# Performance work log

Measured on AMD Instinct MI355X. Metric: run time of the kernel, lower is better.

The kernel has to match this reference:

```python
import jax, jax.numpy as jnp
import numpy as np

N_NODES = 100000
N_EDGES = 3200000
D_IN = 128
UNITS = 128


def setup_inputs() -> dict:
    key = jax.random.key(0)
    k1, k2, k3, k4, k5, k6 = jax.random.split(key, 6)
    x = jax.random.normal(k1, (N_NODES, D_IN), dtype=jnp.float32)
    edge_src = jax.random.randint(k2, (N_EDGES,), 0, N_NODES, dtype=jnp.int32)
    edge_dst = jax.random.randint(k3, (N_EDGES,), 0, N_NODES, dtype=jnp.int32)
    edge_vals = jax.random.uniform(k4, (N_EDGES,), dtype=jnp.float32)
    w = jax.random.normal(k5, (D_IN, UNITS), dtype=jnp.float32) * (2.0 / D_IN) ** 0.5  # he_normal scale
    b = jax.random.normal(k6, (UNITS,), dtype=jnp.float32) * 0.05
    return {"x": x, "edge_src": edge_src, "edge_dst": edge_dst,
            "edge_vals": edge_vals, "w": w, "b": b}


def reference(x, edge_src, edge_dst, edge_vals, w, b):
    # dense transform: [N, D_IN] @ [D_IN, UNITS] -> [N, UNITS]
    h = x @ w
    # sparse adjacency SpMM via edge list: out[dst] += val * h[src]
    msgs = edge_vals[:, None] * h[edge_src]  # [E, UNITS]
    agg = jax.ops.segment_sum(msgs, edge_dst, num_segments=N_NODES)
    # fused bias + relu epilogue
    return jax.nn.relu(agg + b)
```

## Files before the change

### kernel.cpp

```cpp
#include <hip/hip_runtime.h>

#define NODES 100000
#define EDGES 3200000
#define D 128
#define NPB 196
#define NB2 512
#define CH 4096
#define NB_BIN ((EDGES + CH - 1) / CH)
#define CAP 7168
#define MAGIC196 175304788u

typedef unsigned short us8 __attribute__((ext_vector_type(8)));
typedef _Float16 half8 __attribute__((ext_vector_type(8)));
typedef _Float16 h2 __attribute__((ext_vector_type(2)));
typedef float f32x4 __attribute__((ext_vector_type(4)));

__device__ __forceinline__ unsigned short f32_to_f16_bits(float f) {
    return __builtin_bit_cast(unsigned short, (_Float16)f);
}
__device__ __forceinline__ h2 uh2(unsigned u) {
    return __builtin_bit_cast(h2, u);
}
__device__ __forceinline__ int div196(int dst) {
    return (int)(__umulhi((unsigned)dst, MAGIC196) >> 3);
}

__global__ __launch_bounds__(256) void wprep(const float* __restrict__ w,
                                             unsigned short* __restrict__ wt) {
    int i = blockIdx.x * 256 + threadIdx.x;
    if (i >= 16384) return;
    int j  = i & 7;
    int l  = (i >> 3) & 63;
    int c  = (i >> 9) & 3;
    int ct = i >> 11;
    int k   = 32 * c + ((l >> 4) << 3) + j;
    int col = (ct << 4) + (l & 15);
    wt[i] = f32_to_f16_bits(w[k * D + col]);
}

__global__ __launch_bounds__(256) void gemm_mfma(const float* __restrict__ x,
                                                 const unsigned short* __restrict__ wt,
                                                 unsigned short* __restrict__ hb) {
    __shared__ unsigned short wl[16384];
    const int tid = threadIdx.x;
    for (int i = tid; i < 2048; i += 256)
        ((us8*)wl)[i] = ((const us8*)wt)[i];
    __syncthreads();

    const int wave = tid >> 6, lane = tid & 63;
    const long r0 = ((long)blockIdx.x * 4 + wave) * 16;
    if (r0 >= NODES) return;
    const int m = lane & 15, q = lane >> 4;
    const float* xr = x + (r0 + m) * D;

    f32x4 acc[8];
#pragma unroll
    for (int ct = 0; ct < 8; ct++) acc[ct] = (f32x4){0.f, 0.f, 0.f, 0.f};

#pragma unroll
    for (int c = 0; c < 4; c++) {
        const int k0 = 32 * c + 8 * q;
        float4 xa = *(const float4*)(xr + k0);
        float4 xb = *(const float4*)(xr + k0 + 4);
        half8 a;
        a[0] = (_Float16)xa.x;
        a[1] = (_Float16)xa.y;
        a[2] = (_Float16)xa.z;
        a[3] = (_Float16)xa.w;
        a[4] = (_Float16)xb.x;
        a[5] = (_Float16)xb.y;
        a[6] = (_Float16)xb.z;
        a[7] = (_Float16)xb.w;
#pragma unroll
        for (int ct = 0; ct < 8; ct++) {
            half8 bfr = *(const half8*)&wl[(((ct << 2) + c) * 64 + lane) * 8];
            acc[ct] = __builtin_amdgcn_mfma_f32_16x16x32_f16(a, bfr, acc[ct], 0, 0, 0);
        }
    }

#pragma unroll
    for (int ct = 0; ct < 8; ct++) {
#pragma unroll
        for (int r = 0; r < 4; r++) {
            int row = q * 4 + r;
            hb[(r0 + row) * D + ct * 16 + m] = f32_to_f16_bits(acc[ct][r]);
        }
    }
}

__global__ __launch_bounds__(512) void bin_pass1(const int* __restrict__ esrc,
                                                 const int* __restrict__ edst,
                                                 const float* __restrict__ eval,
                                                 int* __restrict__ bcur,
                                                 int2* __restrict__ tmp) {
    __shared__ int2 sed[CH];
    __shared__ int hist[NB2];
    __shared__ int basel[NB2];
    __shared__ int lcur[NB2];
    __shared__ int gbase[NB2];
    __shared__ int wsum[8];
    const int tid = threadIdx.x;
    const long e0 = (long)blockIdx.x * CH;
    const int n = (int)((EDGES - e0 < CH) ? (EDGES - e0) : CH);

    for (int bk = tid; bk < NB2; bk += 512) { hist[bk] = 0; lcur[bk] = 0; }
    __syncthreads();

    unsigned pk[8];
    int ds[8];
#pragma unroll
    for (int u = 0; u < 8; u++) {
        int i = tid + u * 512;
        if (i < n) {
            long e = e0 + i;
            int dst = edst[e];
            int bk = div196(dst);
            int d8 = dst - bk * NPB;
            unsigned hv = (unsigned)f32_to_f16_bits(eval[e]);
            pk[u] = (hv << 17) | (unsigned)esrc[e];
            ds[u] = (bk << 8) | d8;
            atomicAdd(&hist[bk], 1);
        } else {
            ds[u] = -1;
        }
    }
    __syncthreads();

    int h0 = 0, h1 = 0;
    if (tid < 256) { h0 = hist[2 * tid]; h1 = hist[2 * tid + 1]; }
    int s = h0 + h1;
    int lane = tid & 63, wid = tid >> 6;
    int sc = s;
#pragma unroll
    for (int off = 1; off < 64; off <<= 1) {
        int t = __shfl_up(sc, off, 64);
        if (lane >= off) sc += t;
    }
    if (lane == 63) wsum[wid] = sc;
    __syncthreads();
    int wb = 0;
    for (int w2 = 0; w2 < wid && w2 < 4; w2++) wb += wsum[w2];
    int excl = wb + sc - s;
    if (tid < 256) { basel[2 * tid] = excl; basel[2 * tid + 1] = excl + h0; }
    for (int bk = tid; bk < NB2; bk += 512) {
        int c = hist[bk];
        if (c > 0) gbase[bk] = bk * CAP + atomicAdd(&bcur[bk], c);
    }
    __syncthreads();

#pragma unroll
    for (int u = 0; u < 8; u++) {
        if (ds[u] >= 0) {
            int bk = ds[u] >> 8;
            int lp = basel[bk] + atomicAdd(&lcur[bk], 1);
            sed[lp] = make_int2((int)pk[u], ds[u]);
        }
    }
    __syncthreads();

    for (int i = tid; i < n; i += 512) {
        int2 t = sed[i];
        int bk = t.y >> 8;
        tmp[gbase[bk] + (i - basel[bk])] = t;
    }
}

__global__ __launch_bounds__(512) void sort_agg(const int* __restrict__ bcur,
                                                const int2* __restrict__ tmp,
                                                const unsigned short* __restrict__ hb,
                                                const float* __restrict__ bias,
                                                float* __restrict__ out) {
    __shared__ unsigned spk[CAP];
    __shared__ int cnt[256];
    __shared__ int pos[257];
    __shared__ int cur[256];
    __shared__ int wsum[4];
    const int tid = threadIdx.x;
    const int b = blockIdx.x;
    const int n = bcur[b];
    const long base = (long)b * CAP;
    const int lane = tid & 63, wid = tid >> 6;

    if (tid < 256) cnt[tid] = 0;
    __syncthreads();
    for (int i = tid; i < n; i += 512)
        atomicAdd(&cnt[tmp[base + i].y & 255], 1);
    __syncthreads();

    int v = 0, s = 0;
    if (tid < 256) {
        v = cnt[tid];
        s = v;
#pragma unroll
        for (int off = 1; off < 64; off <<= 1) {
            int t = __shfl_up(s, off, 64);
            if (lane >= off) s += t;
        }
        if (lane == 63) wsum[wid] = s;
    }
    __syncthreads();
    if (tid < 256) {
        int wb = 0;
        for (int w2 = 0; w2 < wid; w2++) wb += wsum[w2];
        int excl = wb + s - v;
        pos[tid] = excl;
        cur[tid] = excl;
        if (tid == 255) pos[256] = excl + v;
    }
    __syncthreads();

    for (int i = tid; i < n; i += 512) {
        int2 t = tmp[base + i];
        int p = atomicAdd(&cur[t.y & 255], 1);
        spk[p] = (unsigned)t.x;
    }
    __syncthreads();

    const int sub = lane >> 4, li = lane & 15;
    const unsigned short* hp = hb + li * 8;
    const float* bp = bias + li * 8;
    const float4 b0 = *(const float4*)bp;
    const float4 b1 = *(const float4*)(bp + 4);

    for (int nd = wid; nd < NPB; nd += 8) {
        int node = b * NPB + nd;
        if (node >= NODES) break;
        const int beg = pos[nd], end = pos[nd + 1];

        h2 aA0 = (h2)0, aA1 = (h2)0, aA2 = (h2)0, aA3 = (h2)0;
        h2 aB0 = (h2)0, aB1 = (h2)0, aB2 = (h2)0, aB3 = (h2)0;

        for (int e0 = beg + sub; e0 < end; e0 += 16) {
            int i0 = e0, i1 = e0 + 4, i2 = e0 + 8, i3 = e0 + 12;
            unsigned p0 = spk[i0];
            unsigned p1 = (i1 < end) ? spk[i1] : 0u;
            unsigned p2 = (i2 < end) ? spk[i2] : 0u;
            unsigned p3 = (i3 < end) ? spk[i3] : 0u;

            unsigned s0 = p0 & 0x1FFFFu, s1 = p1 & 0x1FFFFu;
            unsigned s2 = p2 & 0x1FFFFu, s3 = p3 & 0x1FFFFu;
            unsigned v0 = p0 >> 17, v1 = p1 >> 17, v2 = p2 >> 17, v3 = p3 >> 17;

            uint4 r0 = *(const uint4*)(hp + (size_t)s0 * D);
            uint4 r1 = *(const uint4*)(hp + (size_t)s1 * D);
            uint4 r2 = *(const uint4*)(hp + (size_t)s2 * D);
            uint4 r3 = *(const uint4*)(hp + (size_t)s3 * D);

            h2 w0 = uh2(v0 | (v0 << 16));
            h2 w1 = uh2(v1 | (v1 << 16));
            h2 w2 = uh2(v2 | (v2 << 16));
            h2 w3 = uh2(v3 | (v3 << 16));

            aA0 = uh2(r0.x) * w0 + aA0;
            aA1 = uh2(r0.y) * w0 + aA1;
            aA2 = uh2(r0.z) * w0 + aA2;
            aA3 = uh2(r0.w) * w0 + aA3;
            aB0 = uh2(r1.x) * w1 + aB0;
            aB1 = uh2(r1.y) * w1 + aB1;
            aB2 = uh2(r1.z) * w1 + aB2;
            aB3 = uh2(r1.w) * w1 + aB3;
            aA0 = uh2(r2.x) * w2 + aA0;
            aA1 = uh2(r2.y) * w2 + aA1;
            aA2 = uh2(r2.z) * w2 + aA2;
            aA3 = uh2(r2.w) * w2 + aA3;
            aB0 = uh2(r3.x) * w3 + aB0;
            aB1 = uh2(r3.y) * w3 + aB1;
            aB2 = uh2(r3.z) * w3 + aB2;
            aB3 = uh2(r3.w) * w3 + aB3;
        }

        h2 m0 = aA0 + aB0, m1 = aA1 + aB1, m2 = aA2 + aB2, m3 = aA3 + aB3;
        float r[8];
        r[0] = (float)m0[0]; r[1] = (float)m0[1];
        r[2] = (float)m1[0]; r[3] = (float)m1[1];
        r[4] = (float)m2[0]; r[5] = (float)m2[1];
        r[6] = (float)m3[0]; r[7] = (float)m3[1];
#pragma unroll
        for (int k = 0; k < 8; k++) {
            r[k] += __shfl_xor(r[k], 16, 64);
            r[k] += __shfl_xor(r[k], 32, 64);
        }

        if (sub == 0) {
            float4 o0, o1;
            o0.x = fmaxf(r[0] + b0.x, 0.f);
            o0.y = fmaxf(r[1] + b0.y, 0.f);
            o0.z = fmaxf(r[2] + b0.z, 0.f);
            o0.w = fmaxf(r[3] + b0.w, 0.f);
            o1.x = fmaxf(r[4] + b1.x, 0.f);
            o1.y = fmaxf(r[5] + b1.y, 0.f);
            o1.z = fmaxf(r[6] + b1.z, 0.f);
            o1.w = fmaxf(r[7] + b1.w, 0.f);
            float* op = out + (size_t)node * D + li * 8;
            *(float4*)op = o0;
            *(float4*)(op + 4) = o1;
        }
    }
}

extern "C" void kernel_launch(void* const* d_in, const int* in_sizes, int n_in,
                              void* d_out, int out_size, void* d_ws, size_t ws_size,
                              hipStream_t stream) {
    const float* x    = (const float*)d_in[0];
    const int*   esrc = (const int*)  d_in[1];
    const int*   edst = (const int*)  d_in[2];
    const float* eval = (const float*)d_in[3];
    const float* w    = (const float*)d_in[4];
    const float* b    = (const float*)d_in[5];
    float* out = (float*)d_out;

    char* ws = (char*)d_ws;
    const size_t OFF_H    = 0;
    const size_t OFF_WT   = 25600000;
    const size_t OFF_BCUR = OFF_WT   + 32768;
    const size_t OFF_TMP  = OFF_BCUR + 2048;

    unsigned short* hb   = (unsigned short*)(ws + OFF_H);
    unsigned short* wt   = (unsigned short*)(ws + OFF_WT);
    int*            bcur = (int*)           (ws + OFF_BCUR);
    int2*           tmp  = (int2*)          (ws + OFF_TMP);

    hipMemsetAsync(bcur, 0, NB2 * sizeof(int), stream);
    wprep<<<64, 256, 0, stream>>>(w, wt);
    gemm_mfma<<<(NODES + 63) / 64, 256, 0, stream>>>(x, wt, hb);
    bin_pass1<<<NB_BIN, 512, 0, stream>>>(esrc, edst, eval, bcur, tmp);
    sort_agg<<<NB2, 512, 0, stream>>>(bcur, tmp, hb, b, out);
}
```

Before: 286.0 us.

## Fuse weight prep into GEMM, enlarge binning chunks, sort edges by dst and src

```diff
diff --git a/kernel.cpp b/kernel.cpp
--- a/kernel.cpp
+++ b/kernel.cpp
@@ -5,10 +5,11 @@
 #define D 128
 #define NPB 196
 #define NB2 512
-#define CH 4096
+#define CH 8192
 #define NB_BIN ((EDGES + CH - 1) / CH)
 #define CAP 7168
 #define MAGIC196 175304788u
+#define NBIN2 (NPB * 8)
 
 typedef unsigned short us8 __attribute__((ext_vector_type(8)));
 typedef _Float16 half8 __attribute__((ext_vector_type(8)));
@@ -25,30 +26,24 @@
     return (int)(__umulhi((unsigned)dst, MAGIC196) >> 3);
 }
 
-__global__ __launch_bounds__(256) void wprep(const float* __restrict__ w,
-                                             unsigned short* __restrict__ wt) {
-    int i = blockIdx.x * 256 + threadIdx.x;
-    if (i >= 16384) return;
-    int j  = i & 7;
-    int l  = (i >> 3) & 63;
-    int c  = (i >> 9) & 3;
-    int ct = i >> 11;
-    int k   = 32 * c + ((l >> 4) << 3) + j;
-    int col = (ct << 4) + (l & 15);
-    wt[i] = f32_to_f16_bits(w[k * D + col]);
-}
-
-__global__ __launch_bounds__(256) void gemm_mfma(const float* __restrict__ x,
-                                                 const unsigned short* __restrict__ wt,
+__global__ __launch_bounds__(512) void gemm_mfma(const float* __restrict__ x,
+                                                 const float* __restrict__ w,
                                                  unsigned short* __restrict__ hb) {
     __shared__ unsigned short wl[16384];
     const int tid = threadIdx.x;
-    for (int i = tid; i < 2048; i += 256)
-        ((us8*)wl)[i] = ((const us8*)wt)[i];
+    for (int i = tid; i < 16384; i += 512) {
+        int j  = i & 7;
+        int l  = (i >> 3) & 63;
+        int c  = (i >> 9) & 3;
+        int ct = i >> 11;
+        int k   = 32 * c + ((l >> 4) << 3) + j;
+        int col = (ct << 4) + (l & 15);
+        wl[i] = f32_to_f16_bits(w[k * D + col]);
+    }
     __syncthreads();
 
     const int wave = tid >> 6, lane = tid & 63;
-    const long r0 = ((long)blockIdx.x * 4 + wave) * 16;
+    const long r0 = ((long)blockIdx.x * 8 + wave) * 16;
     if (r0 >= NODES) return;
     const int m = lane & 15, q = lane >> 4;
     const float* xr = x + (r0 + m) * D;
@@ -106,10 +101,10 @@
     for (int bk = tid; bk < NB2; bk += 512) { hist[bk] = 0; lcur[bk] = 0; }
     __syncthreads();
 
-    unsigned pk[8];
-    int ds[8];
-#pragma unroll
-    for (int u = 0; u < 8; u++) {
+    unsigned pk[16];
+    int ds[16];
+#pragma unroll
+    for (int u = 0; u < 16; u++) {
         int i = tid + u * 512;
         if (i < n) {
             long e = e0 + i;
@@ -149,7 +144,7 @@
     __syncthreads();
 
 #pragma unroll
-    for (int u = 0; u < 8; u++) {
+    for (int u = 0; u < 16; u++) {
         if (ds[u] >= 0) {
             int bk = ds[u] >> 8;
             int lp = basel[bk] + atomicAdd(&lcur[bk], 1);
@@ -171,47 +166,59 @@
                                                 const float* __restrict__ bias,
                                                 float* __restrict__ out) {
     __shared__ unsigned spk[CAP];
-    __shared__ int cnt[256];
-    __shared__ int pos[257];
-    __shared__ int cur[256];
-    __shared__ int wsum[4];
+    __shared__ int hist[NBIN2];
+    __shared__ int pos[NPB + 1];
+    __shared__ int wsum[8];
     const int tid = threadIdx.x;
     const int b = blockIdx.x;
     const int n = bcur[b];
     const long base = (long)b * CAP;
     const int lane = tid & 63, wid = tid >> 6;
 
-    if (tid < 256) cnt[tid] = 0;
-    __syncthreads();
-    for (int i = tid; i < n; i += 512)
-        atomicAdd(&cnt[tmp[base + i].y & 255], 1);
-    __syncthreads();
-
-    int v = 0, s = 0;
-    if (tid < 256) {
-        v = cnt[tid];
-        s = v;
-#pragma unroll
-        for (int off = 1; off < 64; off <<= 1) {
-            int t = __shfl_up(s, off, 64);
-            if (lane >= off) s += t;
-        }
-        if (lane == 63) wsum[wid] = s;
-    }
-    __syncthreads();
-    if (tid < 256) {
-        int wb = 0;
-        for (int w2 = 0; w2 < wid; w2++) wb += wsum[w2];
-        int excl = wb + s - v;
-        pos[tid] = excl;
-        cur[tid] = excl;
-        if (tid == 255) pos[256] = excl + v;
-    }
+    for (int i = tid; i < NBIN2; i += 512) hist[i] = 0;
     __syncthreads();
 
     for (int i = tid; i < n; i += 512) {
         int2 t = tmp[base + i];
-        int p = atomicAdd(&cur[t.y & 255], 1);
+        int key = ((t.y & 255) << 3) | ((t.x & 0x1FFFF) >> 14);
+        atomicAdd(&hist[key], 1);
+    }
+    __syncthreads();
+
+    int h[4];
+    int s = 0;
+#pragma unroll
+    for (int u = 0; u < 4; u++) {
+        int bi = tid * 4 + u;
+        h[u] = (bi < NBIN2) ? hist[bi] : 0;
+        s += h[u];
+    }
+    int sc = s;
+#pragma unroll
+    for (int off = 1; off < 64; off <<= 1) {
+        int t = __shfl_up(sc, off, 64);
+        if (lane >= off) sc += t;
+    }
+    if (lane == 63) wsum[wid] = sc;
+    __syncthreads();
+    int wb = 0;
+    for (int w2 = 0; w2 < wid; w2++) wb += wsum[w2];
+    int run = wb + sc - s;
+#pragma unroll
+    for (int u = 0; u < 4; u++) {
+        int bi = tid * 4 + u;
+        if (bi < NBIN2) hist[bi] = run;
+        run += h[u];
+    }
+    __syncthreads();
+    if (tid < NPB) pos[tid] = hist[tid << 3];
+    if (tid == NPB) pos[NPB] = n;
+    __syncthreads();
+
+    for (int i = tid; i < n; i += 512) {
+        int2 t = tmp[base + i];
+        int key = ((t.y & 255) << 3) | ((t.x & 0x1FFFF) >> 14);
+        int p = atomicAdd(&hist[key], 1);
         spk[p] = (unsigned)t.x;
     }
     __syncthreads();
@@ -311,18 +318,15 @@
 
     char* ws = (char*)d_ws;
     const size_t OFF_H    = 0;
-    const size_t OFF_WT   = 25600000;
-    const size_t OFF_BCUR = OFF_WT   + 32768;
+    const size_t OFF_BCUR = 25600000;
     const size_t OFF_TMP  = OFF_BCUR + 2048;
 
     unsigned short* hb   = (unsigned short*)(ws + OFF_H);
-    unsigned short* wt   = (unsigned short*)(ws + OFF_WT);
     int*            bcur = (int*)           (ws + OFF_BCUR);
     int2*           tmp  = (int2*)          (ws + OFF_TMP);
 
     hipMemsetAsync(bcur, 0, NB2 * sizeof(int), stream);
-    wprep<<<64, 256, 0, stream>>>(w, wt);
-    gemm_mfma<<<(NODES + 63) / 64, 256, 0, stream>>>(x, wt, hb);
+    gemm_mfma<<<(NODES + 127) / 128, 512, 0, stream>>>(x, w, hb);
     bin_pass1<<<NB_BIN, 512, 0, stream>>>(esrc, edst, eval, bcur, tmp);
     sort_agg<<<NB2, 512, 0, stream>>>(bcur, tmp, hb, b, out);
 }
```

Measured after the change: 280.3 us. 2.0% less time.
